# Kernel optimization log

Measured on AMD Instinct MI355X. Metric: run time of the kernel, lower is better.

## Reference

```python
import jax, jax.numpy as jnp
import numpy as np

D_MODEL = 2048
NHEADS = 16
NOPE = 128
ROPE = 64
VDIM = 128
QLORA = 1536
KVLORA = 512
QHD = NOPE + ROPE  # 192
B, T = 1, 4096


def rms_norm(x, w):
    # torch.nn.RMSNorm with eps=None uses finfo(dtype).eps
    eps = jnp.finfo(x.dtype).eps
    var = jnp.mean(x * x, axis=-1, keepdims=True)
    return x * jax.lax.rsqrt(var + eps) * w


def rope_cos_sin(T, dim):
    freqs = 1.0 / (10000.0 ** (jnp.arange(0, dim, 2, dtype=jnp.float32) / dim))
    ang = jnp.arange(T, dtype=jnp.float32)[:, None] * freqs[None, :]  # (T, dim/2)
    return jnp.cos(ang), jnp.sin(ang)


def apply_rope(x, cos, sin):
    # interleaved RoPE: even/odd channel pairs rotated
    xe = x[..., 0::2]
    xo = x[..., 1::2]
    re = xe * cos - xo * sin
    ro = xo * cos + xe * sin
    return jnp.stack([re, ro], axis=-1).reshape(x.shape)


def setup_inputs() -> dict:
    key = jax.random.key(0)
    ks = jax.random.split(key, 6)
    s = 0.02
    return {
        "x": jax.random.normal(ks[0], (B, T, D_MODEL), jnp.float32),
        "Wqa": jax.random.normal(ks[1], (D_MODEL, QLORA), jnp.float32) * s,
        "q_ln_w": jnp.ones((QLORA,), jnp.float32),
        "Wqb": jax.random.normal(ks[2], (QLORA, NHEADS * QHD), jnp.float32) * s,
        "Wkva": jax.random.normal(ks[3], (D_MODEL, KVLORA + ROPE), jnp.float32) * s,
        "kv_ln_w": jnp.ones((KVLORA,), jnp.float32),
        "Wkvb": jax.random.normal(ks[4], (KVLORA, NHEADS * (NOPE + VDIM)), jnp.float32) * s,
        "Wo": jax.random.normal(ks[5], (NHEADS * VDIM, D_MODEL), jnp.float32) * s,
    }


def reference(x, Wqa, q_ln_w, Wqb, Wkva, kv_ln_w, Wkvb, Wo):
    Bx, Tx, _ = x.shape
    cos, sin = rope_cos_sin(Tx, ROPE)  # (T, ROPE/2)

    # Low-rank Q path
    q = rms_norm(x @ Wqa, q_ln_w) @ Wqb
    q = q.reshape(Bx, Tx, NHEADS, QHD).transpose(0, 2, 1, 3)  # (B,H,T,QHD)
    q_nope = q[..., :NOPE]
    q_rope = apply_rope(q[..., NOPE:], cos, sin)  # (B,H,T,ROPE)

    # Compressed KV path + shared rope key
    kv = x @ Wkva
    kv_c = kv[..., :KVLORA]  # (B,T,KVLORA) latent cache
    k_rope = apply_rope(kv[..., KVLORA:], cos, sin)  # (B,T,ROPE), head-shared

    kvb = (rms_norm(kv_c, kv_ln_w) @ Wkvb).reshape(Bx, Tx, NHEADS, NOPE + VDIM)
    k_nope = kvb[..., :NOPE].transpose(0, 2, 1, 3)  # (B,H,T,NOPE)
    v = kvb[..., NOPE:].transpose(0, 2, 1, 3)       # (B,H,T,VDIM)

    # Scores split into nope part + head-shared rope part (avoids expanding k_rope to H heads)
    scale = 1.0 / jnp.sqrt(jnp.float32(QHD))
    s = jnp.einsum('bhqd,bhkd->bhqk', q_nope, k_nope)
    s = s + jnp.einsum('bhqd,bkd->bhqk', q_rope, k_rope)
    s = s * scale

    mask = jnp.tril(jnp.ones((Tx, Tx), dtype=bool))
    s = jnp.where(mask, s, -jnp.inf)
    a = jax.nn.softmax(s, axis=-1)

    o = jnp.einsum('bhqk,bhkd->bhqd', a, v)
    o = o.transpose(0, 2, 1, 3).reshape(Bx, Tx, NHEADS * VDIM)
    return o @ Wo
```

## Files before the change

kernel.cpp:

```cpp
#include <hip/hip_runtime.h>
#include <hip/hip_bf16.h>

typedef __attribute__((ext_vector_type(8))) short short8;
typedef __attribute__((ext_vector_type(4))) float f32x4;

#define GLDS16(gp, lp)                                                         \
  __builtin_amdgcn_global_load_lds(                                            \
      (const __attribute__((address_space(1))) void*)(gp),                     \
      (__attribute__((address_space(3))) void*)(lp), 16, 0, 0)

static __device__ __forceinline__ unsigned int pack_bf16(float a, float b) {
  __hip_bfloat16 ba = __float2bfloat16(a), bb = __float2bfloat16(b);
  unsigned short ua = *reinterpret_cast<unsigned short*>(&ba);
  unsigned short ub = *reinterpret_cast<unsigned short*>(&bb);
  return (unsigned int)ua | ((unsigned int)ub << 16);
}

static __device__ __forceinline__ int xcd_swz(int linear, int nwg) {
  return (linear & 7) * (nwg >> 3) + (linear >> 3);
}

__global__ __launch_bounds__(256) void cast_bf16_kernel(
    const float* __restrict__ in, __hip_bfloat16* __restrict__ out, int n4)
{
  int i = blockIdx.x * 256 + threadIdx.x;
  if (i < n4) {
    float4 v = ((const float4*)in)[i];
    out[(size_t)i * 4 + 0] = __float2bfloat16(v.x);
    out[(size_t)i * 4 + 1] = __float2bfloat16(v.y);
    out[(size_t)i * 4 + 2] = __float2bfloat16(v.z);
    out[(size_t)i * 4 + 3] = __float2bfloat16(v.w);
  }
}

__global__ void transpose_cast_kernel(const float* __restrict__ in,
                                      __hip_bfloat16* __restrict__ out,
                                      int K, int N, int Npad)
{
  __shared__ float tile[32][33];
  int n0 = blockIdx.x * 32, k0 = blockIdx.y * 32;
  int tx = threadIdx.x, ty = threadIdx.y;
  #pragma unroll
  for (int i = ty; i < 32; i += 8) {
    int k = k0 + i, n = n0 + tx;
    tile[i][tx] = (n < N) ? in[(size_t)k * N + n] : 0.f;
  }
  __syncthreads();
  #pragma unroll
  for (int i = ty; i < 32; i += 8) {
    int n = n0 + i, k = k0 + tx;
    if (n < Npad) out[(size_t)n * K + k] = __float2bfloat16(tile[tx][i]);
  }
}

__global__ void rope_tab_kernel(float* __restrict__ cs, float* __restrict__ sn)
{
  int t = blockIdx.x, i = threadIdx.x;
  float freq = powf(10000.f, -2.f * (float)i / 64.f);
  float ang = (float)t * freq;
  cs[t * 32 + i] = cosf(ang);
  sn[t * 32 + i] = sinf(ang);
}

#define GEMM_MAIN(A, BT, Kdim)                                                 \
  __shared__ __hip_bfloat16 As[128 * 32];                                      \
  __shared__ __hip_bfloat16 Bs[128 * 32];                                      \
  const int tid = threadIdx.x;                                                 \
  const int wave = tid >> 6, lane = tid & 63;                                  \
  const int wr = wave >> 1, wc = wave & 1;                                     \
  const int lq = lane & 15, grp = lane >> 4;                                   \
  const int nwg = gridDim.x * gridDim.y;                                       \
  const int orig = xcd_swz(blockIdx.y * gridDim.x + blockIdx.x, nwg);          \
  const int row0 = (orig / gridDim.x) * 128;                                   \
  const int col0 = (orig % gridDim.x) * 128;                                   \
  const f32x4 z4 = {0.f, 0.f, 0.f, 0.f};                                       \
  f32x4 acc[4][4];                                                             \
  _Pragma("unroll") for (int i = 0; i < 4; i++)                                \
      _Pragma("unroll") for (int j = 0; j < 4; j++) acc[i][j] = z4;            \
  for (int k0 = 0; k0 < (Kdim); k0 += 32) {                                    \
    _Pragma("unroll") for (int i = 0; i < 2; i++) {                            \
      const int t = wave + 4 * i;                                              \
      const int c = t * 64 + lane;                                             \
      const int cr = c >> 2;                                                   \
      const int ko = (c & 3) << 3;                                             \
      GLDS16((A) + (size_t)(row0 + cr) * (Kdim) + (k0 + ko), (char*)As + t * 1024); \
      GLDS16((BT) + (size_t)(col0 + cr) * (Kdim) + (k0 + ko), (char*)Bs + t * 1024);\
    }                                                                          \
    __syncthreads();                                                           \
    short8 af[4], bfr[4];                                                      \
    _Pragma("unroll") for (int mm = 0; mm < 4; mm++)                           \
      af[mm] = *(const short8*)((const short*)As + ((wr * 64 + mm * 16 + lq) * 32 + grp * 8)); \
    _Pragma("unroll") for (int nn = 0; nn < 4; nn++)                           \
      bfr[nn] = *(const short8*)((const short*)Bs + ((wc * 64 + nn * 16 + lq) * 32 + grp * 8));\
    _Pragma("unroll") for (int mm = 0; mm < 4; mm++)                           \
      _Pragma("unroll") for (int nn = 0; nn < 4; nn++)                         \
        acc[mm][nn] = __builtin_amdgcn_mfma_f32_16x16x32_bf16(af[mm], bfr[nn], acc[mm][nn], 0, 0, 0); \
    __syncthreads();                                                           \
  }

__global__ __launch_bounds__(256) void gemm_bt_kernel(
    const __hip_bfloat16* __restrict__ A,
    const __hip_bfloat16* __restrict__ BT,
    float* __restrict__ C, int M, int N, int K)
{
  GEMM_MAIN(A, BT, K)
  #pragma unroll
  for (int mm = 0; mm < 4; mm++)
    #pragma unroll
    for (int nn = 0; nn < 4; nn++) {
      const int row = row0 + wr * 64 + mm * 16 + grp * 4;
      const int col = col0 + wc * 64 + nn * 16 + lq;
      float* Cp = C + (size_t)row * N + col;
      #pragma unroll
      for (int rr = 0; rr < 4; rr++) Cp[(size_t)rr * N] = acc[mm][nn][rr];
    }
}

#define GEMM256_MAIN(Aptr, BTptr, Kdim)                                        \
  __shared__ __align__(16) char Ab[2][32768];                                  \
  __shared__ __align__(16) char Bb[2][32768];                                  \
  const int tid = threadIdx.x;                                                 \
  const int wid = tid >> 6, lane = tid & 63;                                   \
  const int wm = wid >> 2, wn = wid & 3;                                       \
  const int lq = lane & 15, grp = lane >> 4;                                   \
  const int nwg = gridDim.x * gridDim.y;                                       \
  const int orig = xcd_swz(blockIdx.y * gridDim.x + blockIdx.x, nwg);          \
  const int row0 = (orig / gridDim.x) * 256;                                   \
  const int col0 = (orig % gridDim.x) * 256;                                   \
  const size_t K2 = (size_t)(Kdim) * 2;                                        \
  const char* pa[4]; const char* pb[4]; int ldst[4];                           \
  _Pragma("unroll") for (int i = 0; i < 4; i++) {                              \
    int L = i * 8192 + tid * 16;                                               \
    int r = L >> 7;                                                            \
    int csw = (L & 127) ^ ((r & 7) << 4);                                      \
    ldst[i] = L;                                                               \
    pa[i] = (const char*)(Aptr) + (size_t)(row0 + r) * K2 + csw;               \
    pb[i] = (const char*)(BTptr) + (size_t)(col0 + r) * K2 + csw;              \
  }                                                                            \
  const int xm = (lq & 7) << 4;                                                \
  const f32x4 z4 = {0.f, 0.f, 0.f, 0.f};                                       \
  f32x4 acc[8][4];                                                             \
  _Pragma("unroll") for (int i = 0; i < 8; i++)                                \
    _Pragma("unroll") for (int j = 0; j < 4; j++) acc[i][j] = z4;              \
  const int nt = (Kdim) >> 6;                                                  \
  _Pragma("unroll") for (int i = 0; i < 4; i++) {                              \
    GLDS16(pa[i], &Ab[0][0] + ldst[i]);                                        \
    GLDS16(pb[i], &Bb[0][0] + ldst[i]);                                        \
  }                                                                            \
  for (int t = 0; t < nt; ++t) {                                               \
    const int b = t & 1;                                                       \
    if (t + 1 < nt) {                                                          \
      const size_t koff = (size_t)(t + 1) * 128;                               \
      _Pragma("unroll") for (int i = 0; i < 4; i++) {                          \
        GLDS16(pa[i] + koff, &Ab[b ^ 1][0] + ldst[i]);                         \
        GLDS16(pb[i] + koff, &Bb[b ^ 1][0] + ldst[i]);                         \
      }                                                                        \
      asm volatile("s_waitcnt vmcnt(8)" ::: "memory");                         \
    } else {                                                                   \
      asm volatile("s_waitcnt vmcnt(0)" ::: "memory");                         \
    }                                                                          \
    __builtin_amdgcn_sched_barrier(0);                                         \
    __builtin_amdgcn_s_barrier();             \
    __builtin_amdgcn_sched_barrier(0);                                         \
    const char* Ar = &Ab[b][0];                                                \
    const char* Br = &Bb[b][0];                                                \
    short8 bfr[4][2];                                                          \
    _Pragma("unroll") for (int n = 0; n < 4; n++)                              \
      _Pragma("unroll") for (int ks = 0; ks < 2; ks++)                         \
        bfr[n][ks] = *(const short8*)(Br + (wn * 64 + n * 16 + lq) * 128 +     \
                                      ((ks * 64 + grp * 16) ^ xm));            \
    _Pragma("unroll") for (int mh = 0; mh < 4; mh++) {                         \
      short8 af[2][2];                                                         \
      _Pragma("unroll") for (int mi = 0; mi < 2; mi++)                         \
        _Pragma("unroll") for (int ks = 0; ks < 2; ks++)                       \
          af[mi][ks] = *(const short8*)(Ar + (wm * 128 + (mh * 2 + mi) * 16 + lq) * 128 + \
                                        ((ks * 64 + grp * 16) ^ xm));          \
      __builtin_amdgcn_s_setprio(1);                                           \
      _Pragma("unroll") for (int mi = 0; mi < 2; mi++)                         \
        _Pragma("unroll") for (int n = 0; n < 4; n++)                          \
          _Pragma("unroll") for (int ks = 0; ks < 2; ks++)                     \
            acc[mh * 2 + mi][n] = __builtin_amdgcn_mfma_f32_16x16x32_bf16(     \
                af[mi][ks], bfr[n][ks], acc[mh * 2 + mi][n], 0, 0, 0);         \
      __builtin_amdgcn_s_setprio(0);                                           \
    }                                                                          \
    __builtin_amdgcn_sched_barrier(0);                                         \
    __builtin_amdgcn_s_barrier();             \
    __builtin_amdgcn_sched_barrier(0);                                         \
  }

__global__ __launch_bounds__(512, 2) void gemm256_bt_kernel(
    const __hip_bfloat16* __restrict__ A,
    const __hip_bfloat16* __restrict__ BT,
    float* __restrict__ C, int N, int K)
{
  GEMM256_MAIN(A, BT, K)
  #pragma unroll
  for (int m = 0; m < 8; m++)
    #pragma unroll
    for (int n = 0; n < 4; n++) {
      const int row = row0 + wm * 128 + m * 16 + grp * 4;
      const int col = col0 + wn * 64 + n * 16 + lq;
      float* Cp = C + (size_t)row * N + col;
      #pragma unroll
      for (int rr = 0; rr < 4; rr++) Cp[(size_t)rr * N] = acc[m][n][rr];
    }
}

__global__ __launch_bounds__(512, 2) void gemm256_qup_kernel(
    const __hip_bfloat16* __restrict__ A,
    const __hip_bfloat16* __restrict__ BT,
    __hip_bfloat16* __restrict__ Qh,
    const float* __restrict__ cs_tab, const float* __restrict__ sn_tab, int K)
{
  GEMM256_MAIN(A, BT, K)
  const float scale = 0.10411654209f;
  #pragma unroll
  for (int m = 0; m < 8; m++)
    #pragma unroll
    for (int n = 0; n < 4; n++) {
      const int col = col0 + wn * 64 + n * 16 + lq;
      const int h = col / 192;
      const int d = col - h * 192;
      const bool is_rope = (d >= 128);
      const int i = (d - 128) >> 1;
      const float sgn = (d & 1) ? 1.f : -1.f;
      #pragma unroll
      for (int rr = 0; rr < 4; rr++) {
        const int t = row0 + wm * 128 + m * 16 + grp * 4 + rr;
        float val = acc[m][n][rr];
        float partner = __shfl_xor(val, 1);
        float outv = val;
        if (is_rope) {
          float c = cs_tab[t * 32 + i];
          float s = sn_tab[t * 32 + i];
          outv = val * c + sgn * partner * s;
        }
        Qh[((size_t)h * 4096 + t) * 192 + d] = __float2bfloat16(outv * scale);
      }
    }
}

__global__ __launch_bounds__(512, 2) void gemm256_kvup_kernel(
    const __hip_bfloat16* __restrict__ A,
    const __hip_bfloat16* __restrict__ BT,
    __hip_bfloat16* __restrict__ Kh,
    __hip_bfloat16* __restrict__ Vt, int K)
{
  GEMM256_MAIN(A, BT, K)
  #pragma unroll
  for (int m = 0; m < 8; m++)
    #pragma unroll
    for (int n = 0; n < 4; n++) {
      const int col = col0 + wn * 64 + n * 16 + lq;
      const int h = col >> 8;
      const int j = col & 255;
      const int t0 = row0 + wm * 128 + m * 16 + grp * 4;
      if (j < 128) {
        #pragma unroll
        for (int rr = 0; rr < 4; rr++)
          Kh[((size_t)h * 4096 + t0 + rr) * 192 + j] = __float2bfloat16(acc[m][n][rr]);
      } else {
        const int vd = j - 128;
        uint2 w;
        w.x = pack_bf16(acc[m][n][0], acc[m][n][1]);
        w.y = pack_bf16(acc[m][n][2], acc[m][n][3]);
        *(uint2*)(Vt + ((size_t)h * 128 + vd) * 4096 + t0) = w;
      }
    }
}

__global__ __launch_bounds__(256) void rmsnorm_cast_kernel(
    const float* __restrict__ in, int ld_in, const float* __restrict__ w,
    __hip_bfloat16* __restrict__ out, int W)
{
  const int row = blockIdx.x;
  const int tid = threadIdx.x;
  const int wave = tid >> 6, lane = tid & 63;
  const float* x = in + (size_t)row * ld_in;
  float ss = 0.f;
  for (int i = tid; i < W; i += 256) { float v = x[i]; ss += v * v; }
  #pragma unroll
  for (int o = 32; o; o >>= 1) ss += __shfl_xor(ss, o);
  __shared__ float red[4];
  __shared__ float stot;
  if (lane == 0) red[wave] = ss;
  __syncthreads();
  if (tid == 0) stot = red[0] + red[1] + red[2] + red[3];
  __syncthreads();
  const float rstd = rsqrtf(stot / (float)W + 1.1920929e-7f);
  for (int i = tid; i < W; i += 256)
    out[(size_t)row * W + i] = __float2bfloat16(x[i] * rstd * w[i]);
}

__global__ void rope_k_kernel(const float* __restrict__ kv, __hip_bfloat16* __restrict__ kr)
{
  int t = blockIdx.x;
  int i = threadIdx.x;
  if (i < 32) {
    float freq = powf(10000.f, -2.f * (float)i / 64.f);
    float ang = (float)t * freq;
    float c = cosf(ang), s = sinf(ang);
    float xe = kv[(size_t)t * 640 + 512 + 2 * i];
    float xo = kv[(size_t)t * 640 + 512 + 2 * i + 1];
    kr[(size_t)t * 64 + 2 * i]     = __float2bfloat16(xe * c - xo * s);
    kr[(size_t)t * 64 + 2 * i + 1] = __float2bfloat16(xo * c + xe * s);
  }
}

__global__ __launch_bounds__(256) void prep_krope_kernel(
    const __hip_bfloat16* __restrict__ kr, __hip_bfloat16* __restrict__ Kh)
{
  const int t = blockIdx.x;
  const int tid = threadIdx.x;
  for (int e = tid; e < 1024; e += 256) {
    int h = e >> 6, d = e & 63;
    Kh[((size_t)h * 4096 + t) * 192 + 128 + d] = kr[(size_t)t * 64 + d];
  }
}

__global__ __launch_bounds__(256, 2) void flash_attn_kernel(
    const __hip_bfloat16* __restrict__ Qh,
    const __hip_bfloat16* __restrict__ Kh,
    const __hip_bfloat16* __restrict__ Vt,
    __hip_bfloat16* __restrict__ Obf)
{
  __shared__ __align__(16) char Klds[2][24576];
  __shared__ __align__(16) char Vlds[2][16384];

  const int hw = blockIdx.x;
  const int rest = hw >> 3;
  const int h = (hw & 7) + 8 * (rest & 1);
  const int p = rest >> 1;

  const int wave = threadIdx.x >> 6;
  const int lane = threadIdx.x & 63;
  const int lq = lane & 15;
  const int grp = lane >> 4;
  const int qb_[2] = {(63 - p) * 64 + wave * 16,
                      p * 64 + wave * 16};
  const int kendA = qb_[0] + 16;
  const int kendB = qb_[1] + 16;
  const int nt = 64 - p;

  const char* Kh_ = (const char*)(Kh + (size_t)h * 4096 * 192);
  const char* Vh_ = (const char*)(Vt + (size_t)h * 128 * 4096);
  const short* Qh_ = (const short*)Qh + (size_t)h * 4096 * 192;

  int kbase[6], vbase[4];
  #pragma unroll
  for (int i = 0; i < 6; i++) {
    int L = (wave * 6 + i) * 1024 + lane * 16;
    int r = L / 384, c = L - r * 384;
    int swb = (r & 3) | (((r >> 3) & 1) << 2);
    kbase[i] = r * 384 + (c ^ (swb << 4));
  }
  #pragma unroll
  for (int i = 0; i < 4; i++) {
    int L = (wave * 4 + i) * 1024 + lane * 16;
    int r = L >> 7, c = L & 127;
    vbase[i] = r * 8192 + (c ^ ((r & 7) << 4));
  }

  short8 qf[2][6];
  #pragma unroll
  for (int f = 0; f < 2; f++)
    #pragma unroll
    for (int d = 0; d < 6; d++)
      qf[f][d] = *(const short8*)(Qh_ + (size_t)(qb_[f] + lq) * 192 + d * 32 + grp * 8);

  const f32x4 z4 = {0.f, 0.f, 0.f, 0.f};
  f32x4 o_acc[2][8];
  #pragma unroll
  for (int f = 0; f < 2; f++)
    #pragma unroll
    for (int v = 0; v < 8; v++) o_acc[f][v] = z4;
  float m[2] = {-1e30f, -1e30f};
  float lsum[2] = {0.f, 0.f};

  const int krow_l = ((lq >> 2) << 3) + (lq & 3);
  const int kxm = ((lq & 3) | (((lq >> 2) & 1) << 2)) << 4;
  const int vxm = (lq & 7) << 4;

  {
    #pragma unroll
    for (int i = 0; i < 6; i++) GLDS16(Kh_ + kbase[i], Klds[0] + (wave * 6 + i) * 1024);
    #pragma unroll
    for (int i = 0; i < 4; i++) GLDS16(Vh_ + vbase[i], Vlds[0] + (wave * 4 + i) * 1024);
  }

  for (int t = 0; t < nt; t++) {
    __syncthreads();
    if (t + 1 < nt) {
      const char* Kp = Kh_ + (size_t)(t + 1) * 64 * 384;
      const char* Vp = Vh_ + (size_t)(t + 1) * 128;
      char* Kd = Klds[(t + 1) & 1];
      char* Vd = Vlds[(t + 1) & 1];
      #pragma unroll
      for (int i = 0; i < 6; i++) GLDS16(Kp + kbase[i], Kd + (wave * 6 + i) * 1024);
      #pragma unroll
      for (int i = 0; i < 4; i++) GLDS16(Vp + vbase[i], Vd + (wave * 4 + i) * 1024);
    }
    const char* Kb = Klds[t & 1];
    const char* Vb = Vlds[t & 1];
    const int ks = t * 64;

    #pragma unroll
    for (int h2 = 0; h2 < 2; h2++) {
      const int ks32 = ks + h2 * 32;
      if (ks32 >= kendA) continue;
      const bool act1 = (ks32 < kendB);

      f32x4 st[2][2];
      #pragma unroll
      for (int kt = 0; kt < 2; kt++) {
        const int row = h2 * 32 + krow_l + kt * 4;
        short8 kf[6];
        #pragma unroll
        for (int d = 0; d < 6; d++)
          kf[d] = *(const short8*)(Kb + row * 384 + ((d * 64 + grp * 16) ^ kxm));
        #pragma unroll
        for (int f = 0; f < 2; f++) {
          if (f == 1 && !act1) continue;
          f32x4 acc = z4;
          #pragma unroll
          for (int d = 0; d < 6; d++)
            acc = __builtin_amdgcn_mfma_f32_16x16x32_bf16(kf[d], qf[f][d], acc, 0, 0, 0);
          st[f][kt] = acc;
        }
      }

      short8 vf[8];
      #pragma unroll
      for (int v = 0; v < 8; v++)
        vf[v] = *(const short8*)(Vb + (v * 16 + lq) * 128 + ((h2 * 64 + grp * 16) ^ vxm));

      #pragma unroll
      for (int f = 0; f < 2; f++) {
        if (f == 1 && !act1) continue;
        const int qg = qb_[f] + lq;
        const bool need_mask = (ks32 + 31 > qb_[f]);
        if (need_mask) {
          #pragma unroll
          for (int kt = 0; kt < 2; kt++)
            #pragma unroll
            for (int r = 0; r < 4; r++) {
              int key = ks32 + grp * 8 + kt * 4 + r;
              if (key > qg) st[f][kt][r] = -1e30f;
            }
        }
        float tmax = fmaxf(fmaxf(fmaxf(st[f][0][0], st[f][0][1]), fmaxf(st[f][0][2], st[f][0][3])),
                           fmaxf(fmaxf(st[f][1][0], st[f][1][1]), fmaxf(st[f][1][2], st[f][1][3])));
        tmax = fmaxf(tmax, __shfl_xor(tmax, 16));
        tmax = fmaxf(tmax, __shfl_xor(tmax, 32));
        if (!__all(tmax <= m[f] + 11.5416f)) {
          float mnew = fmaxf(m[f], tmax);
          float alpha = exp2f(m[f] - mnew);
          m[f] = mnew;
          lsum[f] *= alpha;
          float a0 = __shfl(alpha, grp * 4 + 0);
          float a1 = __shfl(alpha, grp * 4 + 1);
          float a2 = __shfl(alpha, grp * 4 + 2);
          float a3 = __shfl(alpha, grp * 4 + 3);
          #pragma unroll
          for (int v = 0; v < 8; v++) {
            o_acc[f][v][0] *= a0; o_acc[f][v][1] *= a1;
            o_acc[f][v][2] *= a2; o_acc[f][v][3] *= a3;
          }
        }
        float p00 = exp2f(st[f][0][0] - m[f]), p01 = exp2f(st[f][0][1] - m[f]);
        float p02 = exp2f(st[f][0][2] - m[f]), p03 = exp2f(st[f][0][3] - m[f]);
        float p10 = exp2f(st[f][1][0] - m[f]), p11 = exp2f(st[f][1][1] - m[f]);
        float p12 = exp2f(st[f][1][2] - m[f]), p13 = exp2f(st[f][1][3] - m[f]);
        float psum = ((p00 + p01) + (p02 + p03)) + ((p10 + p11) + (p12 + p13));
        psum += __shfl_xor(psum, 16);
        psum += __shfl_xor(psum, 32);
        lsum[f] += psum;
        union { unsigned int u[4]; short8 s8; } pu;
        pu.u[0] = pack_bf16(p00, p01);
        pu.u[1] = pack_bf16(p02, p03);
        pu.u[2] = pack_bf16(p10, p11);
        pu.u[3] = pack_bf16(p12, p13);
        short8 pa = pu.s8;
        #pragma unroll
        for (int v = 0; v < 8; v++)
          o_acc[f][v] = __builtin_amdgcn_mfma_f32_16x16x32_bf16(pa, vf[v], o_acc[f][v], 0, 0, 0);
      }
    }
  }

  #pragma unroll
  for (int f = 0; f < 2; f++) {
    float linv = 1.f / lsum[f];
    float l0 = __shfl(linv, grp * 4 + 0);
    float l1 = __shfl(linv, grp * 4 + 1);
    float l2 = __shfl(linv, grp * 4 + 2);
    float l3 = __shfl(linv, grp * 4 + 3);
    const int qb = qb_[f];
    #pragma unroll
    for (int v = 0; v < 8; v++) {
      int col = h * 128 + v * 16 + lq;
      Obf[(size_t)(qb + grp * 4 + 0) * 2048 + col] = __float2bfloat16(o_acc[f][v][0] * l0);
      Obf[(size_t)(qb + grp * 4 + 1) * 2048 + col] = __float2bfloat16(o_acc[f][v][1] * l1);
      Obf[(size_t)(qb + grp * 4 + 2) * 2048 + col] = __float2bfloat16(o_acc[f][v][2] * l2);
      Obf[(size_t)(qb + grp * 4 + 3) * 2048 + col] = __float2bfloat16(o_acc[f][v][3] * l3);
    }
  }
}

extern "C" void kernel_launch(void* const* d_in, const int* in_sizes, int n_in,
                              void* d_out, int out_size, void* d_ws, size_t ws_size,
                              hipStream_t stream)
{
  (void)in_sizes; (void)n_in; (void)out_size; (void)ws_size;
  const float* x     = (const float*)d_in[0];
  const float* Wqa   = (const float*)d_in[1];
  const float* qlnw  = (const float*)d_in[2];
  const float* Wqb   = (const float*)d_in[3];
  const float* Wkva  = (const float*)d_in[4];
  const float* kvlnw = (const float*)d_in[5];
  const float* Wkvb  = (const float*)d_in[6];
  const float* Wo    = (const float*)d_in[7];
  float* out = (float*)d_out;
  char* ws = (char*)d_ws;

  size_t off = 0;
  auto take = [&](size_t bytes) {
    char* p = ws + off;
    off += (bytes + 255) & ~(size_t)255;
    return p;
  };

  __hip_bfloat16* x_bf  = (__hip_bfloat16*)take((size_t)4096 * 2048 * 2);
  __hip_bfloat16* WqaT  = (__hip_bfloat16*)take((size_t)1536 * 2048 * 2);
  __hip_bfloat16* WqbT  = (__hip_bfloat16*)take((size_t)3072 * 1536 * 2);
  __hip_bfloat16* WkvaT = (__hip_bfloat16*)take((size_t)640 * 2048 * 2);
  __hip_bfloat16* WkvbT = (__hip_bfloat16*)take((size_t)4096 * 512 * 2);
  __hip_bfloat16* WoT   = (__hip_bfloat16*)take((size_t)2048 * 2048 * 2);
  char* regA            = take((size_t)4096 * 1536 * 4);
  float* kv             = (float*)take((size_t)4096 * 640 * 4);
  __hip_bfloat16* q_ln  = (__hip_bfloat16*)take((size_t)4096 * 1536 * 2);
  __hip_bfloat16* kv_ln = (__hip_bfloat16*)take((size_t)4096 * 512 * 2);
  __hip_bfloat16* kr    = (__hip_bfloat16*)take((size_t)4096 * 64 * 2);
  float* cs_tab         = (float*)take((size_t)4096 * 32 * 4);
  float* sn_tab         = (float*)take((size_t)4096 * 32 * 4);
  __hip_bfloat16* Khp   = (__hip_bfloat16*)take((size_t)16 * 4096 * 192 * 2);
  __hip_bfloat16* Vtp   = (__hip_bfloat16*)take((size_t)16 * 128 * 4096 * 2);
  __hip_bfloat16* o_bf  = (__hip_bfloat16*)take((size_t)4096 * 2048 * 2);

  float* q_lat = (float*)regA;
  __hip_bfloat16* Qh = (__hip_bfloat16*)regA;

  cast_bf16_kernel<<<dim3(8192), 256, 0, stream>>>(x, x_bf, 2097152);
  transpose_cast_kernel<<<dim3(48, 64), dim3(32, 8), 0, stream>>>(Wqa, WqaT, 2048, 1536, 1536);
  transpose_cast_kernel<<<dim3(96, 48), dim3(32, 8), 0, stream>>>(Wqb, WqbT, 1536, 3072, 3072);
  transpose_cast_kernel<<<dim3(20, 64), dim3(32, 8), 0, stream>>>(Wkva, WkvaT, 2048, 576, 640);
  transpose_cast_kernel<<<dim3(128, 16), dim3(32, 8), 0, stream>>>(Wkvb, WkvbT, 512, 4096, 4096);
  transpose_cast_kernel<<<dim3(64, 64), dim3(32, 8), 0, stream>>>(Wo, WoT, 2048, 2048, 2048);
  rope_tab_kernel<<<dim3(4096), 32, 0, stream>>>(cs_tab, sn_tab);

  gemm_bt_kernel<<<dim3(12, 32), 256, 0, stream>>>(x_bf, WqaT, q_lat, 4096, 1536, 2048);
  gemm_bt_kernel<<<dim3(5, 32), 256, 0, stream>>>(x_bf, WkvaT, kv, 4096, 640, 2048);

  rmsnorm_cast_kernel<<<dim3(4096), 256, 0, stream>>>(q_lat, 1536, qlnw, q_ln, 1536);
  rmsnorm_cast_kernel<<<dim3(4096), 256, 0, stream>>>(kv, 640, kvlnw, kv_ln, 512);
  rope_k_kernel<<<dim3(4096), 64, 0, stream>>>(kv, kr);

  gemm256_qup_kernel<<<dim3(12, 16), 512, 0, stream>>>(q_ln, WqbT, Qh, cs_tab, sn_tab, 1536);
  gemm256_kvup_kernel<<<dim3(16, 16), 512, 0, stream>>>(kv_ln, WkvbT, Khp, Vtp, 512);
  prep_krope_kernel<<<dim3(4096), 256, 0, stream>>>(kr, Khp);

  flash_attn_kernel<<<dim3(512), 256, 0, stream>>>(Qh, Khp, Vtp, o_bf);

  gemm256_bt_kernel<<<dim3(8, 16), 512, 0, stream>>>(o_bf, WoT, out, 2048, 2048);
}
```

Before: 479.9 us.

## Merge down-projection GEMMs, fuse RMSNorm with K rope, defer softmax row-sum reduction

```diff
diff --git a/kernel.cpp b/kernel.cpp
--- a/kernel.cpp
+++ b/kernel.cpp
@@ -98,21 +98,23 @@
     __syncthreads();                                                           \
   }
 
-__global__ __launch_bounds__(256) void gemm_bt_kernel(
+__global__ __launch_bounds__(256) void gemm_down_kernel(
     const __hip_bfloat16* __restrict__ A,
     const __hip_bfloat16* __restrict__ BT,
-    float* __restrict__ C, int M, int N, int K)
-{
-  GEMM_MAIN(A, BT, K)
+    float* __restrict__ q_lat, float* __restrict__ kvout)
+{
+  GEMM_MAIN(A, BT, 2048)
   #pragma unroll
   for (int mm = 0; mm < 4; mm++)
     #pragma unroll
     for (int nn = 0; nn < 4; nn++) {
       const int row = row0 + wr * 64 + mm * 16 + grp * 4;
       const int col = col0 + wc * 64 + nn * 16 + lq;
-      float* Cp = C + (size_t)row * N + col;
-      #pragma unroll
-      for (int rr = 0; rr < 4; rr++) Cp[(size_t)rr * N] = acc[mm][nn][rr];
+      float* Cp = (col < 1536) ? (q_lat + (size_t)row * 1536 + col)
+                               : (kvout + (size_t)row * 640 + (col - 1536));
+      const size_t ld = (col < 1536) ? 1536 : 640;
+      #pragma unroll
+      for (int rr = 0; rr < 4; rr++) Cp[(size_t)rr * ld] = acc[mm][nn][rr];
     }
 }
 
@@ -269,14 +271,23 @@
     }
 }
 
-__global__ __launch_bounds__(256) void rmsnorm_cast_kernel(
-    const float* __restrict__ in, int ld_in, const float* __restrict__ w,
-    __hip_bfloat16* __restrict__ out, int W)
-{
-  const int row = blockIdx.x;
+__global__ __launch_bounds__(256) void rmsnorm2_kernel(
+    const float* __restrict__ q_lat, const float* __restrict__ kv,
+    const float* __restrict__ qw, const float* __restrict__ kvw,
+    __hip_bfloat16* __restrict__ q_ln, __hip_bfloat16* __restrict__ kv_ln,
+    const float* __restrict__ cs_tab, const float* __restrict__ sn_tab,
+    __hip_bfloat16* __restrict__ Kh)
+{
+  const int b = blockIdx.x;
+  const bool isq = (b < 4096);
+  const int row = isq ? b : b - 4096;
+  const int ld = isq ? 1536 : 640;
+  const int W = isq ? 1536 : 512;
+  const float* x = (isq ? q_lat : kv) + (size_t)row * ld;
+  const float* w = isq ? qw : kvw;
+  __hip_bfloat16* out = (isq ? q_ln : kv_ln) + (size_t)row * W;
   const int tid = threadIdx.x;
   const int wave = tid >> 6, lane = tid & 63;
-  const float* x = in + (size_t)row * ld_in;
   float ss = 0.f;
   for (int i = tid; i < W; i += 256) { float v = x[i]; ss += v * v; }
   #pragma unroll
@@ -289,32 +300,18 @@
   __syncthreads();
   const float rstd = rsqrtf(stot / (float)W + 1.1920929e-7f);
   for (int i = tid; i < W; i += 256)
-    out[(size_t)row * W + i] = __float2bfloat16(x[i] * rstd * w[i]);
-}
-
-__global__ void rope_k_kernel(const float* __restrict__ kv, __hip_bfloat16* __restrict__ kr)
-{
-  int t = blockIdx.x;
-  int i = threadIdx.x;
-  if (i < 32) {
-    float freq = powf(10000.f, -2.f * (float)i / 64.f);
-    float ang = (float)t * freq;
-    float c = cosf(ang), s = sinf(ang);
-    float xe = kv[(size_t)t * 640 + 512 + 2 * i];
-    float xo = kv[(size_t)t * 640 + 512 + 2 * i + 1];
-    kr[(size_t)t * 64 + 2 * i]     = __float2bfloat16(xe * c - xo * s);
-    kr[(size_t)t * 64 + 2 * i + 1] = __float2bfloat16(xo * c + xe * s);
-  }
-}
-
-__global__ __launch_bounds__(256) void prep_krope_kernel(
-    const __hip_bfloat16* __restrict__ kr, __hip_bfloat16* __restrict__ Kh)
-{
-  const int t = blockIdx.x;
-  const int tid = threadIdx.x;
-  for (int e = tid; e < 1024; e += 256) {
-    int h = e >> 6, d = e & 63;
-    Kh[((size_t)h * 4096 + t) * 192 + 128 + d] = kr[(size_t)t * 64 + d];
+    out[i] = __float2bfloat16(x[i] * rstd * w[i]);
+  if (!isq) {
+    const int t = row;
+    for (int e = tid; e < 512; e += 256) {
+      int h = e >> 5, i = e & 31;
+      float c = cs_tab[t * 32 + i], s = sn_tab[t * 32 + i];
+      float xe = x[512 + 2 * i];
+      float xo = x[512 + 2 * i + 1];
+      size_t base = ((size_t)h * 4096 + t) * 192 + 128 + 2 * i;
+      Kh[base]     = __float2bfloat16(xe * c - xo * s);
+      Kh[base + 1] = __float2bfloat16(xo * c + xe * s);
+    }
   }
 }
 
@@ -471,10 +468,7 @@
         float p02 = exp2f(st[f][0][2] - m[f]), p03 = exp2f(st[f][0][3] - m[f]);
         float p10 = exp2f(st[f][1][0] - m[f]), p11 = exp2f(st[f][1][1] - m[f]);
         float p12 = exp2f(st[f][1][2] - m[f]), p13 = exp2f(st[f][1][3] - m[f]);
-        float psum = ((p00 + p01) + (p02 + p03)) + ((p10 + p11) + (p12 + p13));
-        psum += __shfl_xor(psum, 16);
-        psum += __shfl_xor(psum, 32);
-        lsum[f] += psum;
+        lsum[f] += ((p00 + p01) + (p02 + p03)) + ((p10 + p11) + (p12 + p13));
         union { unsigned int u[4]; short8 s8; } pu;
         pu.u[0] = pack_bf16(p00, p01);
         pu.u[1] = pack_bf16(p02, p03);
@@ -490,7 +484,10 @@
 
   #pragma unroll
   for (int f = 0; f < 2; f++) {
-    float linv = 1.f / lsum[f];
+    float ls = lsum[f];
+    ls += __shfl_xor(ls, 16);
+    ls += __shfl_xor(ls, 32);
+    float linv = 1.f / ls;
     float l0 = __shfl(linv, grp * 4 + 0);
     float l1 = __shfl(linv, grp * 4 + 1);
     float l2 = __shfl(linv, grp * 4 + 2);
@@ -530,44 +527,39 @@
     return p;
   };
 
-  __hip_bfloat16* x_bf  = (__hip_bfloat16*)take((size_t)4096 * 2048 * 2);
-  __hip_bfloat16* WqaT  = (__hip_bfloat16*)take((size_t)1536 * 2048 * 2);
-  __hip_bfloat16* WqbT  = (__hip_bfloat16*)take((size_t)3072 * 1536 * 2);
-  __hip_bfloat16* WkvaT = (__hip_bfloat16*)take((size_t)640 * 2048 * 2);
-  __hip_bfloat16* WkvbT = (__hip_bfloat16*)take((size_t)4096 * 512 * 2);
-  __hip_bfloat16* WoT   = (__hip_bfloat16*)take((size_t)2048 * 2048 * 2);
-  char* regA            = take((size_t)4096 * 1536 * 4);
-  float* kv             = (float*)take((size_t)4096 * 640 * 4);
-  __hip_bfloat16* q_ln  = (__hip_bfloat16*)take((size_t)4096 * 1536 * 2);
-  __hip_bfloat16* kv_ln = (__hip_bfloat16*)take((size_t)4096 * 512 * 2);
-  __hip_bfloat16* kr    = (__hip_bfloat16*)take((size_t)4096 * 64 * 2);
-  float* cs_tab         = (float*)take((size_t)4096 * 32 * 4);
-  float* sn_tab         = (float*)take((size_t)4096 * 32 * 4);
-  __hip_bfloat16* Khp   = (__hip_bfloat16*)take((size_t)16 * 4096 * 192 * 2);
-  __hip_bfloat16* Vtp   = (__hip_bfloat16*)take((size_t)16 * 128 * 4096 * 2);
-  __hip_bfloat16* o_bf  = (__hip_bfloat16*)take((size_t)4096 * 2048 * 2);
+  __hip_bfloat16* x_bf   = (__hip_bfloat16*)take((size_t)4096 * 2048 * 2);
+  __hip_bfloat16* WdownT = (__hip_bfloat16*)take((size_t)2176 * 2048 * 2);
+  __hip_bfloat16* WqbT   = (__hip_bfloat16*)take((size_t)3072 * 1536 * 2);
+  __hip_bfloat16* WkvbT  = (__hip_bfloat16*)take((size_t)4096 * 512 * 2);
+  __hip_bfloat16* WoT    = (__hip_bfloat16*)take((size_t)2048 * 2048 * 2);
+  char* regA             = take((size_t)4096 * 1536 * 4);
+  float* kv              = (float*)take((size_t)4096 * 640 * 4);
+  __hip_bfloat16* q_ln   = (__hip_bfloat16*)take((size_t)4096 * 1536 * 2);
+  __hip_bfloat16* kv_ln  = (__hip_bfloat16*)take((size_t)4096 * 512 * 2);
+  float* cs_tab          = (float*)take((size_t)4096 * 32 * 4);
+  float* sn_tab          = (float*)take((size_t)4096 * 32 * 4);
+  __hip_bfloat16* Khp    = (__hip_bfloat16*)take((size_t)16 * 4096 * 192 * 2);
+  __hip_bfloat16* Vtp    = (__hip_bfloat16*)take((size_t)16 * 128 * 4096 * 2);
+  __hip_bfloat16* o_bf   = (__hip_bfloat16*)take((size_t)4096 * 2048 * 2);
 
   float* q_lat = (float*)regA;
   __hip_bfloat16* Qh = (__hip_bfloat16*)regA;
 
   cast_bf16_kernel<<<dim3(8192), 256, 0, stream>>>(x, x_bf, 2097152);
-  transpose_cast_kernel<<<dim3(48, 64), dim3(32, 8), 0, stream>>>(Wqa, WqaT, 2048, 1536, 1536);
+  transpose_cast_kernel<<<dim3(48, 64), dim3(32, 8), 0, stream>>>(Wqa, WdownT, 2048, 1536, 1536);
+  transpose_cast_kernel<<<dim3(20, 64), dim3(32, 8), 0, stream>>>(Wkva, WdownT + (size_t)1536 * 2048, 2048, 576, 640);
   transpose_cast_kernel<<<dim3(96, 48), dim3(32, 8), 0, stream>>>(Wqb, WqbT, 1536, 3072, 3072);
-  transpose_cast_kernel<<<dim3(20, 64), dim3(32, 8), 0, stream>>>(Wkva, WkvaT, 2048, 576, 640);
   transpose_cast_kernel<<<dim3(128, 16), dim3(32, 8), 0, stream>>>(Wkvb, WkvbT, 512, 4096, 4096);
   transpose_cast_kernel<<<dim3(64, 64), dim3(32, 8), 0, stream>>>(Wo, WoT, 2048, 2048, 2048);
   rope_tab_kernel<<<dim3(4096), 32, 0, stream>>>(cs_tab, sn_tab);
 
-  gemm_bt_kernel<<<dim3(12, 32), 256, 0, stream>>>(x_bf, WqaT, q_lat, 4096, 1536, 2048);
-  gemm_bt_kernel<<<dim3(5, 32), 256, 0, stream>>>(x_bf, WkvaT, kv, 4096, 640, 2048);
-
-  rmsnorm_cast_kernel<<<dim3(4096), 256, 0, stream>>>(q_lat, 1536, qlnw, q_ln, 1536);
-  rmsnorm_cast_kernel<<<dim3(4096), 256, 0, stream>>>(kv, 640, kvlnw, kv_ln, 512);
-  rope_k_kernel<<<dim3(4096), 64, 0, stream>>>(kv, kr);
+  gemm_down_kernel<<<dim3(17, 32), 256, 0, stream>>>(x_bf, WdownT, q_lat, kv);
+
+  rmsnorm2_kernel<<<dim3(8192), 256, 0, stream>>>(q_lat, kv, qlnw, kvlnw, q_ln, kv_ln,
+                                                  cs_tab, sn_tab, Khp);
 
   gemm256_qup_kernel<<<dim3(12, 16), 512, 0, stream>>>(q_ln, WqbT, Qh, cs_tab, sn_tab, 1536);
   gemm256_kvup_kernel<<<dim3(16, 16), 512, 0, stream>>>(kv_ln, WkvbT, Khp, Vtp, 512);
-  prep_krope_kernel<<<dim3(4096), 256, 0, stream>>>(kr, Khp);
 
   flash_attn_kernel<<<dim3(512), 256, 0, stream>>>(Qh, Khp, Vtp, o_bf);
 
```

Result: faster. 466.3 us (-2.8%).
